# Kernel tuning notes

Measured on AMD Instinct MI355X. Metric: run time of the kernel, lower is better.

The kernel has to match this reference:

```python
import jax, jax.numpy as jnp
from jax import lax
import numpy as np

K = 8          # local window radius -> (2K+1)^2 = 289 offsets
TOPK = 256     # topk channels kept for fg/bg correlation
EPS = 1e-5     # torch InstanceNorm2d default eps


def _conv3(x, w, b):
    # 3x3 conv, stride 1, pad 1, NCHW/OIHW
    y = lax.conv_general_dilated(x, w, (1, 1), ((1, 1), (1, 1)),
                                 dimension_numbers=('NCHW', 'OIHW', 'NCHW'))
    return y + b[None, :, None, None]


def _inorm(x):
    # InstanceNorm2d(affine=False): per (b,c) normalization over HxW, biased var
    m = jnp.mean(x, axis=(2, 3), keepdims=True)
    v = jnp.mean((x - m) ** 2, axis=(2, 3), keepdims=True)
    return (x - m) * lax.rsqrt(v + EPS)


def _aic(x, w1, b1, w2, b2):
    # AIC(in, hidden): conv3x3(in->hidden)+IN+ReLU -> conv3x3(hidden->in)+IN+ReLU
    h = jax.nn.relu(_inorm(_conv3(x, w1, b1)))
    return jax.nn.relu(_inorm(_conv3(h, w2, b2)))


def _amaxpool(x, H, W):
    # adaptive_max_pool2d with exact integer factor (384/48 = 8)
    kh, kw = x.shape[2] // H, x.shape[3] // W
    return lax.reduce_window(x, -jnp.inf, lax.max, (1, 1, kh, kw), (1, 1, kh, kw), 'VALID')


def _topk_c(x, k=TOPK):
    # topk over channel axis, values sorted descending (matches torch.topk)
    v, _ = lax.top_k(jnp.transpose(x, (0, 2, 3, 1)), k)  # [B,H,W,k]
    return jnp.transpose(v, (0, 3, 1, 2))                 # [B,k,H,W]


def _resize_ac(x, H, W):
    # bilinear interpolate, align_corners=True
    B, C, h, w = x.shape
    def grid(n_out, n_in):
        if n_out == 1:
            return jnp.zeros((1,), jnp.float32)
        return jnp.arange(n_out, dtype=jnp.float32) * ((n_in - 1) / (n_out - 1))
    ys, xs = grid(H, h), grid(W, w)
    y0 = jnp.clip(jnp.floor(ys).astype(jnp.int32), 0, h - 1)
    y1 = jnp.minimum(y0 + 1, h - 1)
    x0 = jnp.clip(jnp.floor(xs).astype(jnp.int32), 0, w - 1)
    x1 = jnp.minimum(x0 + 1, w - 1)
    wy = (ys - y0.astype(jnp.float32))[None, None, :, None]
    wx = (xs - x0.astype(jnp.float32))[None, None, None, :]
    rows = x[:, :, y0, :] * (1.0 - wy) + x[:, :, y1, :] * wy  # [B,C,H,w]
    return rows[:, :, :, x0] * (1.0 - wx) + rows[:, :, :, x1] * wx


def _forward(p3, p2, p1, kg1, klp, key_mask, pre_mask,
             conv_top_w, conv_top_b,
             aic_top_w1, aic_top_b1, aic_top_w2, aic_top_b2,
             r1a_w1, r1a_b1, r1a_w2, r1a_b2,
             r1b_w1, r1b_b1, r1b_w2, r1b_b2,
             r2a_w1, r2a_b1, r2a_w2, r2a_b2,
             r2b_w1, r2b_b1, r2b_w2, r2b_b2,
             dec_conv1_w, dec_conv1_b, pred_w, pred_b):
    B, _, H, W = kg1.shape  # kg1: [B, H*W, H, W]
    # --- Global, mode=2: fg/bg topk over the global correlation volume ---
    gm = _amaxpool(key_mask, H, W).reshape(B, H * W, 1, 1)
    gf = _topk_c(kg1 * gm)
    gb = _topk_c(kg1 * (1.0 - gm))
    # --- Local, mode=2: unfold mask into 17x17 windows, fg/bg topk ---
    lm = _amaxpool(pre_mask, H, W)                       # [B,1,H,W]
    lmp = jnp.pad(lm, ((0, 0), (0, 0), (K, K), (K, K)))  # zero pad (FF.pad default)
    patches = lax.conv_general_dilated_patches(
        lmp, (2 * K + 1, 2 * K + 1), (1, 1), 'VALID',
        dimension_numbers=('NCHW', 'OIHW', 'NCHW'))      # [B,289,H,W], ch = dy*17+dx
    lf = _topk_c(klp * patches)
    lb = _topk_c(klp * (1.0 - patches))
    # --- fuse at p3 resolution ---
    pm = _amaxpool(pre_mask, H, W)
    x = jnp.concatenate([p3, gf, gb, lf, lb, pm], axis=1)  # [B, 256*5+1, H, W]
    x = _conv3(x, conv_top_w, conv_top_b)                  # 1281 -> 256
    x = _aic(x, aic_top_w1, aic_top_b1, aic_top_w2, aic_top_b2)
    # --- Decoder: Refine(256,64) -> conv 256->64 -> Refine(64,64) -> pred ---
    y = _resize_ac(x, p2.shape[2], p2.shape[3])
    y = _aic(y, r1a_w1, r1a_b1, r1a_w2, r1a_b2)
    y = y + p2
    y = _aic(y, r1b_w1, r1b_b1, r1b_w2, r1b_b2)
    y = _conv3(y, dec_conv1_w, dec_conv1_b)
    z = _resize_ac(y, p1.shape[2], p1.shape[3])
    z = _aic(z, r2a_w1, r2a_b1, r2a_w2, r2a_b2)
    z = z + p1
    z = _aic(z, r2b_w1, r2b_b1, r2b_w2, r2b_b2)
    return jax.nn.sigmoid(_conv3(z, pred_w, pred_b))       # [B,1,192,192]


def setup_inputs() -> dict:
    key = jax.random.key(0)
    ks = jax.random.split(key, 40)
    B, H, W = 2, 48, 48
    inp = {}
    inp['p3'] = jax.random.normal(ks[0], (B, 256, H, W), jnp.float32)
    inp['p2'] = jax.random.normal(ks[1], (B, 256, 2 * H, 2 * W), jnp.float32)
    inp['p1'] = jax.random.normal(ks[2], (B, 64, 4 * H, 4 * W), jnp.float32)
    inp['kg1'] = jax.random.normal(ks[3], (B, H * W, H, W), jnp.float32)
    inp['klp'] = jax.random.normal(ks[4], (B, (2 * K + 1) ** 2, H, W), jnp.float32)
    inp['key_mask'] = jax.random.uniform(ks[5], (B, 1, 8 * H, 8 * W), dtype=jnp.float32)
    inp['pre_mask'] = jax.random.uniform(ks[6], (B, 1, 8 * H, 8 * W), dtype=jnp.float32)
    i = [7]
    def p(shape, s=0.05):
        w = jax.random.normal(ks[i[0]], shape, jnp.float32) * s
        i[0] += 1
        return w
    inp['conv_top_w'] = p((256, 256 * 5 + 1, 3, 3))
    inp['conv_top_b'] = jnp.zeros((256,), jnp.float32)
    for nm, (ci, ch) in [('aic_top', (256, 64)), ('r1a', (256, 64)), ('r1b', (256, 64)),
                         ('r2a', (64, 64)), ('r2b', (64, 64))]:
        inp[nm + '_w1'] = p((ch, ci, 3, 3)); inp[nm + '_b1'] = jnp.zeros((ch,), jnp.float32)
        inp[nm + '_w2'] = p((ci, ch, 3, 3)); inp[nm + '_b2'] = jnp.zeros((ci,), jnp.float32)
    inp['dec_conv1_w'] = p((64, 256, 3, 3)); inp['dec_conv1_b'] = jnp.zeros((64,), jnp.float32)
    inp['pred_w'] = p((1, 64, 3, 3)); inp['pred_b'] = jnp.zeros((1,), jnp.float32)
    return inp


def reference(p3, p2, p1, kg1, klp, key_mask, pre_mask,
              conv_top_w, conv_top_b,
              aic_top_w1, aic_top_b1, aic_top_w2, aic_top_b2,
              r1a_w1, r1a_b1, r1a_w2, r1a_b2,
              r1b_w1, r1b_b1, r1b_w2, r1b_b2,
              r2a_w1, r2a_b1, r2a_w2, r2a_b2,
              r2b_w1, r2b_b1, r2b_w2, r2b_b2,
              dec_conv1_w, dec_conv1_b, pred_w, pred_b):
    return _forward(p3, p2, p1, kg1, klp, key_mask, pre_mask,
                    conv_top_w, conv_top_b,
                    aic_top_w1, aic_top_b1, aic_top_w2, aic_top_b2,
                    r1a_w1, r1a_b1, r1a_w2, r1a_b2,
                    r1b_w1, r1b_b1, r1b_w2, r1b_b2,
                    r2a_w1, r2a_b1, r2a_w2, r2a_b2,
                    r2b_w1, r2b_b1, r2b_w2, r2b_b2,
                    dec_conv1_w, dec_conv1_b, pred_w, pred_b)
```

## Files before the change

kernel.cpp:

```cpp
#include <hip/hip_runtime.h>
#include <math.h>

#define TPB 256

typedef _Float16 h8 __attribute__((ext_vector_type(8)));
typedef float f4 __attribute__((ext_vector_type(4)));
typedef unsigned short ushort_t;

__device__ __forceinline__ unsigned short f2bf(float x) {
  unsigned int u = __float_as_uint(x);
  unsigned int r = (u + 0x7fffu + ((u >> 16) & 1u)) >> 16;
  return (unsigned short)r;
}
__device__ __forceinline__ float bf2f(unsigned short h) {
  return __uint_as_float(((unsigned int)h) << 16);
}
__device__ __forceinline__ ushort_t f2h(float x) {
  _Float16 h = (_Float16)x;
  return *(ushort_t*)&h;
}
__device__ __forceinline__ float h2f(ushort_t u) {
  _Float16 h = *(_Float16*)&u;
  return (float)h;
}
__device__ __forceinline__ unsigned key_of(float x) {
  unsigned u = __float_as_uint(x);
  return u ^ ((u >> 31) ? 0xFFFFFFFFu : 0x80000000u);
}
__device__ __forceinline__ float un_key(unsigned k) {
  unsigned u = k ^ ((k >> 31) ? 0x80000000u : 0xFFFFFFFFu);
  return __uint_as_float(u);
}

__global__ __launch_bounds__(TPB) void pool8_kernel(const float* __restrict__ in,
                                                    float* __restrict__ out, int total) {
  int idx = blockIdx.x * TPB + threadIdx.x;
  if (idx >= total) return;
  int b = idx / 2304, yx = idx - b * 2304;
  int y = yx / 48, x = yx - y * 48;
  const float* p = in + ((size_t)b * 384 + (size_t)y * 8) * 384 + (size_t)x * 8;
  float m = -INFINITY;
#pragma unroll
  for (int i = 0; i < 8; ++i)
#pragma unroll
    for (int j = 0; j < 8; ++j) m = fmaxf(m, p[(size_t)i * 384 + j]);
  out[idx] = m;
}

__global__ __launch_bounds__(TPB) void tposef_kernel(const float* __restrict__ src,
                                                     float* __restrict__ dst, int C, int HW,
                                                     int DS) {
  __shared__ float tile[64][65];
  int px0 = blockIdx.x * 64;
  int c0 = blockIdx.y * 64;
  int b = blockIdx.z;
  int tid = threadIdx.x;
#pragma unroll
  for (int i = 0; i < 16; ++i) {
    int c = (tid >> 6) + i * 4, p = tid & 63;
    tile[c][p] = src[((size_t)b * C + c0 + c) * HW + px0 + p];
  }
  __syncthreads();
#pragma unroll
  for (int i = 0; i < 16; ++i) {
    int c = tid & 63, p = (tid >> 6) + i * 4;
    dst[((size_t)b * HW + px0 + p) * DS + c0 + c] = tile[c][p];
  }
}

__global__ __launch_bounds__(TPB) void tposeg_kernel(const float* __restrict__ src,
                                                     float* __restrict__ dst, int C, int HW,
                                                     int DS) {
  __shared__ float tile[64][65];
  int px0 = blockIdx.x * 64;
  int c0 = blockIdx.y * 64;
  int b = blockIdx.z;
  int tid = threadIdx.x;
#pragma unroll
  for (int i = 0; i < 16; ++i) {
    int c = (tid >> 6) + i * 4, p = tid & 63;
    float v = 0.f;
    if (c0 + c < C) v = src[((size_t)b * C + c0 + c) * HW + px0 + p];
    tile[c][p] = v;
  }
  __syncthreads();
#pragma unroll
  for (int i = 0; i < 16; ++i) {
    int c = tid & 63, p = (tid >> 6) + i * 4;
    if (c0 + c < C)
      dst[((size_t)b * HW + px0 + p) * DS + c0 + c] = tile[c][p];
  }
}

__global__ __launch_bounds__(TPB) void tposeh_kernel(const float* __restrict__ src,
                                                     ushort_t* __restrict__ dst, int C, int HW,
                                                     int DS) {
  __shared__ float tile[64][65];
  int px0 = blockIdx.x * 64;
  int c0 = blockIdx.y * 64;
  int b = blockIdx.z;
  int tid = threadIdx.x;
#pragma unroll
  for (int i = 0; i < 16; ++i) {
    int c = (tid >> 6) + i * 4, p = tid & 63;
    tile[c][p] = src[((size_t)b * C + c0 + c) * HW + px0 + p];
  }
  __syncthreads();
#pragma unroll
  for (int i = 0; i < 16; ++i) {
    int c = tid & 63, p = (tid >> 6) + i * 4;
    dst[((size_t)b * HW + px0 + p) * DS + c0 + c] = f2h(tile[c][p]);
  }
}

__global__ __launch_bounds__(TPB) void topk_global_kernel(const float* __restrict__ kgT,
                                                          const float* __restrict__ gm,
                                                          ushort_t* __restrict__ xcat) {
  __shared__ unsigned histF[256], histB[256];
  __shared__ unsigned soutF[256], soutB[256];
  __shared__ unsigned selT[2], selA[2];
  __shared__ unsigned cntG[2], cntE[2];
  const int tid = threadIdx.x;
  const int lane = tid & 63, wid = tid >> 6;
  int bid = blockIdx.x;
  int b = bid / 2304, yx = bid - b * 2304;
  const float* kp = kgT + ((size_t)b * 2304 + yx) * 2304;
  const float* gp = gm + (size_t)b * 2304;
  unsigned kF[9], kB[9];
#pragma unroll
  for (int j = 0; j < 9; ++j) {
    int i = tid + 256 * j;
    float v = kp[i];
    float g = gp[i];
    kF[j] = key_of(v * g);
    kB[j] = key_of(v * (1.0f - g));
  }
  unsigned prefF = 0, prefB = 0;
  unsigned KF = 256, KB = 256;
  unsigned gtF = 0, gtB = 0;
#pragma unroll
  for (int p = 0; p < 4; ++p) {
    const int shift = 24 - 8 * p;
    histF[tid] = 0;
    histB[tid] = 0;
    __syncthreads();
#pragma unroll
    for (int j = 0; j < 9; ++j) {
      if (p == 0 || (kF[j] >> (shift + 8)) == prefF)
        atomicAdd(&histF[(kF[j] >> shift) & 0xFFu], 1u);
      if (p == 0 || (kB[j] >> (shift + 8)) == prefB)
        atomicAdd(&histB[(kB[j] >> shift) & 0xFFu], 1u);
    }
    __syncthreads();
    if (wid < 2) {
      unsigned* h = wid ? histB : histF;
      unsigned K = wid ? KB : KF;
      unsigned h0 = h[4 * lane], h1 = h[4 * lane + 1];
      unsigned h2 = h[4 * lane + 2], h3 = h[4 * lane + 3];
      unsigned x = h0 + h1 + h2 + h3;
#pragma unroll
      for (int d = 1; d < 64; d <<= 1) {
        unsigned y = __shfl_down(x, d, 64);
        if (lane + d < 64) x += y;
      }
      unsigned long long m = __ballot(x >= K);
      int tl = 63 - __clzll(m);
      if (lane == tl) {
        unsigned s1 = x - h0, s2 = s1 - h1, s3 = s2 - h2, s4 = s3 - h3;
        int jj;
        unsigned A;
        if (s3 >= K) { jj = 3; A = s4; }
        else if (s2 >= K) { jj = 2; A = s3; }
        else if (s1 >= K) { jj = 1; A = s2; }
        else { jj = 0; A = s1; }
        selT[wid] = 4 * tl + jj;
        selA[wid] = A;
      }
    }
    __syncthreads();
    unsigned TF = selT[0], AF = selA[0];
    unsigned TB = selT[1], AB = selA[1];
    prefF = (prefF << 8) | TF; gtF += AF; KF -= AF;
    prefB = (prefB << 8) | TB; gtB += AB; KB -= AB;
    __syncthreads();
  }
  const unsigned tF = prefF, tB = prefB;
  const unsigned nGTF = gtF, needF = KF;
  const unsigned nGTB = gtB, needB = KB;
  if (tid == 0) { cntG[0] = 0; cntG[1] = 0; cntE[0] = 0; cntE[1] = 0; }
  __syncthreads();
#pragma unroll
  for (int j = 0; j < 9; ++j) {
    unsigned k = kF[j];
    if (k > tF) soutF[atomicAdd(&cntG[0], 1u)] = k;
    else if (k == tF) {
      unsigned e = atomicAdd(&cntE[0], 1u);
      if (e < needF) soutF[nGTF + e] = tF;
    }
    k = kB[j];
    if (k > tB) soutB[atomicAdd(&cntG[1], 1u)] = k;
    else if (k == tB) {
      unsigned e = atomicAdd(&cntE[1], 1u);
      if (e < needB) soutB[nGTB + e] = tB;
    }
  }
  __syncthreads();
  if (wid < 2) {
    unsigned* sarr = wid ? soutB : soutF;
    for (int kk = 2; kk <= 256; kk <<= 1) {
      for (int j = kk >> 1; j > 0; j >>= 1) {
#pragma unroll
        for (int r = 0; r < 2; ++r) {
          int p = lane + r * 64;
          int t = (p & (j - 1)) | ((p & ~(j - 1)) << 1);
          int ixj = t | j;
          bool up = ((t & kk) == 0);
          unsigned a = sarr[t], c = sarr[ixj];
          if (up ? (a > c) : (a < c)) { sarr[t] = c; sarr[ixj] = a; }
        }
        __builtin_amdgcn_wave_barrier();
      }
    }
  }
  __syncthreads();
  size_t base = ((size_t)(b * 2304 + yx)) * 1312;
  xcat[base + 256 + tid] = f2h(un_key(soutF[255 - tid]));
  xcat[base + 512 + tid] = f2h(un_key(soutB[255 - tid]));
}

__global__ __launch_bounds__(64) void topk_local_kernel(const float* __restrict__ klpT,
                                                        const float* __restrict__ lm,
                                                        ushort_t* __restrict__ xcat) {
  __shared__ float sf[512];
  __shared__ float sb[512];
  const int lane = threadIdx.x;
  const int pix = blockIdx.x;
  const int b = pix / 2304;
  const int yx = pix - b * 2304;
  const int y = yx / 48, x = yx - y * 48;
  const float* kp = klpT + (size_t)pix * 320;
#pragma unroll
  for (int r = 0; r < 8; ++r) {
    int i = lane + r * 64;
    float vf = -INFINITY, vb = -INFINITY;
    if (i < 289) {
      int dy = i / 17, dx = i - dy * 17;
      int sy = y + dy - 8, sx = x + dx - 8;
      float pv = 0.f;
      if (sy >= 0 && sy < 48 && sx >= 0 && sx < 48) pv = lm[(size_t)b * 2304 + sy * 48 + sx];
      float v = kp[i];
      vf = v * pv;
      vb = v * (1.0f - pv);
    }
    sf[i] = vf;
    sb[i] = vb;
  }
  __builtin_amdgcn_wave_barrier();
  for (int k = 2; k <= 512; k <<= 1) {
    for (int j = k >> 1; j > 0; j >>= 1) {
#pragma unroll
      for (int r = 0; r < 4; ++r) {
        int p = lane + r * 64;
        int t = (p & (j - 1)) | ((p & ~(j - 1)) << 1);
        int ixj = t | j;
        bool up = ((t & k) == 0);
        float a = sf[t], c = sf[ixj];
        if (up ? (a > c) : (a < c)) { sf[t] = c; sf[ixj] = a; }
        a = sb[t]; c = sb[ixj];
        if (up ? (a > c) : (a < c)) { sb[t] = c; sb[ixj] = a; }
      }
      __builtin_amdgcn_wave_barrier();
    }
  }
  size_t base = (size_t)pix * 1312;
#pragma unroll
  for (int r = 0; r < 4; ++r) {
    int t = lane + r * 64;
    xcat[base + 768 + t] = f2h(sf[511 - t]);
    xcat[base + 1024 + t] = f2h(sb[511 - t]);
  }
}

__global__ __launch_bounds__(TPB) void pm_pad_kernel(const float* __restrict__ lm,
                                                     ushort_t* __restrict__ xcat) {
  int idx = blockIdx.x * TPB + threadIdx.x;
  if (idx >= 2 * 2304 * 32) return;
  int ch = idx & 31;
  int r = idx >> 5;
  xcat[(size_t)r * 1312 + 1280 + ch] = (ch == 0) ? f2h(lm[r]) : (ushort_t)0;
}

struct WallDesc {
  const float* src[13];
  int CinW[13], CIP[13], CoutPad[13], CoutReal[13];
  unsigned start[14];
  int n;
};
__global__ __launch_bounds__(TPB) void wconv_all_kernel(WallDesc D, ushort_t* __restrict__ whi,
                                                        int total) {
  int i = blockIdx.x * TPB + threadIdx.x;
  if (i >= total) return;
  int k = 0;
  while (k + 1 < D.n && (unsigned)i >= D.start[k + 1]) ++k;
  int j = i - D.start[k];
  int e = j & 7;
  int t = j >> 3;
  int l16 = t & 15; t >>= 4;
  int h4 = t & 3; t >>= 2;
  int NCOG = D.CoutPad[k] >> 4;
  int cog = t % NCOG; t /= NCOG;
  int kykx = t % 9;
  int chunk = t / 9;
  int co = cog * 16 + l16;
  int ci = chunk * 32 + h4 * 8 + e;
  float v = 0.f;
  if (ci < D.CinW[k] && co < D.CoutReal[k])
    v = D.src[k][((size_t)co * D.CinW[k] + ci) * 9 + kykx];
  whi[i] = f2h(v);
}

template <int NORM>
__device__ __forceinline__ uint4 norm8(uint4 v, const float* __restrict__ nmean,
                                       const float* __restrict__ ninv,
                                       const void* __restrict__ nres, size_t mb,
                                       size_t pxoff) {
  float f[8];
  f[0] = h2f((ushort_t)(v.x & 0xffff)); f[1] = h2f((ushort_t)(v.x >> 16));
  f[2] = h2f((ushort_t)(v.y & 0xffff)); f[3] = h2f((ushort_t)(v.y >> 16));
  f[4] = h2f((ushort_t)(v.z & 0xffff)); f[5] = h2f((ushort_t)(v.z >> 16));
  f[6] = h2f((ushort_t)(v.w & 0xffff)); f[7] = h2f((ushort_t)(v.w >> 16));
  float4 m0 = *(const float4*)(nmean + mb);
  float4 m1 = *(const float4*)(nmean + mb + 4);
  float4 i0 = *(const float4*)(ninv + mb);
  float4 i1 = *(const float4*)(ninv + mb + 4);
  float o[8];
  o[0] = fmaxf((f[0] - m0.x) * i0.x, 0.f);
  o[1] = fmaxf((f[1] - m0.y) * i0.y, 0.f);
  o[2] = fmaxf((f[2] - m0.z) * i0.z, 0.f);
  o[3] = fmaxf((f[3] - m0.w) * i0.w, 0.f);
  o[4] = fmaxf((f[4] - m1.x) * i1.x, 0.f);
  o[5] = fmaxf((f[5] - m1.y) * i1.y, 0.f);
  o[6] = fmaxf((f[6] - m1.z) * i1.z, 0.f);
  o[7] = fmaxf((f[7] - m1.w) * i1.w, 0.f);
  if (NORM == 2) {
    uint4 rv = *(const uint4*)((const ushort_t*)nres + pxoff);
    o[0] += h2f((ushort_t)(rv.x & 0xffff)); o[1] += h2f((ushort_t)(rv.x >> 16));
    o[2] += h2f((ushort_t)(rv.y & 0xffff)); o[3] += h2f((ushort_t)(rv.y >> 16));
    o[4] += h2f((ushort_t)(rv.z & 0xffff)); o[5] += h2f((ushort_t)(rv.z >> 16));
    o[6] += h2f((ushort_t)(rv.w & 0xffff)); o[7] += h2f((ushort_t)(rv.w >> 16));
  } else if (NORM == 3) {
    const float* rp = (const float*)nres + pxoff;
    float4 r0 = *(const float4*)rp;
    float4 r1 = *(const float4*)(rp + 4);
    o[0] += r0.x; o[1] += r0.y; o[2] += r0.z; o[3] += r0.w;
    o[4] += r1.x; o[5] += r1.y; o[6] += r1.z; o[7] += r1.w;
  }
  uint4 out;
  out.x = (unsigned)f2h(o[0]) | ((unsigned)f2h(o[1]) << 16);
  out.y = (unsigned)f2h(o[2]) | ((unsigned)f2h(o[3]) << 16);
  out.z = (unsigned)f2h(o[4]) | ((unsigned)f2h(o[5]) << 16);
  out.w = (unsigned)f2h(o[6]) | ((unsigned)f2h(o[7]) << 16);
  return out;
}

template <int MFR, int ACT, int STAT, int GEOM, int NORM>
__global__ __launch_bounds__(TPB) void conv_mfma_kernel(
    const ushort_t* __restrict__ in, const ushort_t* __restrict__ whi,
    const float* __restrict__ bias,
    ushort_t* __restrict__ outh, float* __restrict__ outf, ushort_t* __restrict__ partial,
    float* __restrict__ stat, int ntiles,
    const float* __restrict__ nmean, const float* __restrict__ ninv,
    const void* __restrict__ nres,
    int hin, int win, float rs,
    int CIP, int Cout, int H, int W, int S, int ci_per_s) {
  const int NPIX = (GEOM == 1) ? 100 : 180;
  const int PITCH = 10;
  __shared__ uint4 sB[(GEOM == 1) ? 800 : 1440];
  const int MB = (GEOM == 1) ? 64 : MFR * 32;
  const int tid = threadIdx.x;
  const int lane = tid & 63;
  const int lo16 = lane & 15, hi4 = lane >> 4;
  const int wid = tid >> 6;
  const int wco = (GEOM == 1) ? wid : (wid & 1);
  const int wpx = (GEOM == 1) ? 0 : (wid >> 1);
  const int tilesX = W >> 3;
  const int tx0 = (blockIdx.x % tilesX) << 3;
  const int ty0 = (blockIdx.x / tilesX) << ((GEOM == 1) ? 3 : 4);
  const int s = blockIdx.y % S;
  const int co0 = (blockIdx.y / S) * MB;
  const int b = blockIdx.z;
  const int NCOG = Cout >> 4;
  const size_t HW = (size_t)H * W;
  const ushort_t* inb = in + (size_t)b * HW * CIP;
  const ushort_t* srcb = in + (size_t)b * hin * win * CIP;
  int ci_begin = s * ci_per_s;
  int ci_end = ci_begin + ci_per_s;
  if (ci_end > CIP) ci_end = CIP;
  f4 acc[MFR][4];
#pragma unroll
  for (int m = 0; m < MFR; ++m)
#pragma unroll
    for (int n = 0; n < 4; ++n) acc[m][n] = (f4){0.f, 0.f, 0.f, 0.f};

  for (int ci0 = ci_begin; ci0 < ci_end; ci0 += 64) {
    const bool has2 = (ci0 + 32 < ci_end);
    __syncthreads();
#pragma unroll
    for (int it = 0; it < 6; ++it) {
      int u = it * TPB + tid;
      if (u < NPIX * 8) {
        int q4 = u / NPIX;
        int pix = u - q4 * NPIX;
        int prow = pix / PITCH, pcol = pix - prow * PITCH;
        int gy = ty0 - 1 + prow, gx = tx0 - 1 + pcol;
        int ci = ci0 + q4 * 8;
        bool inbp = (ci < CIP && gy >= 0 && gy < H && gx >= 0 && gx < W);
        uint4 v = {0u, 0u, 0u, 0u};
        if (inbp) {
          if (NORM <= 3) {
            v = *(const uint4*)(inb + ((size_t)gy * W + gx) * CIP + ci);
            if (NORM != 0) {
              size_t mb = (size_t)b * CIP + ci;
              size_t pxoff = ((size_t)b * HW + (size_t)gy * W + gx) * CIP + ci;
              v = norm8<NORM>(v, nmean, ninv, nres, mb, pxoff);
            }
          } else {
            float ys = gy * rs, xs = gx * rs;
            int y0 = (int)floorf(ys);
            if (y0 > hin - 1) y0 = hin - 1;
            int x0 = (int)floorf(xs);
            if (x0 > win - 1) x0 = win - 1;
            int y1 = y0 + 1 < hin ? y0 + 1 : hin - 1;
            int x1 = x0 + 1 < win ? x0 + 1 : win - 1;
            float wy = ys - (float)y0, wx = xs - (float)x0;
            uint4 s00 = *(const uint4*)(srcb + ((size_t)y0 * win + x0) * CIP + ci);
            uint4 s01 = *(const uint4*)(srcb + ((size_t)y0 * win + x1) * CIP + ci);
            uint4 s10 = *(const uint4*)(srcb + ((size_t)y1 * win + x0) * CIP + ci);
            uint4 s11 = *(const uint4*)(srcb + ((size_t)y1 * win + x1) * CIP + ci);
            float w00 = (1.f - wy) * (1.f - wx), w01 = (1.f - wy) * wx;
            float w10 = wy * (1.f - wx), w11 = wy * wx;
            union U8 { uint4 q; ushort_t sv[8]; };
            U8 u00, u01, u10, u11, uo;
            u00.q = s00; u01.q = s01; u10.q = s10; u11.q = s11;
#pragma unroll
            for (int k8 = 0; k8 < 8; ++k8) {
              float val = h2f(u00.sv[k8]) * w00 + h2f(u01.sv[k8]) * w01 +
                          h2f(u10.sv[k8]) * w10 + h2f(u11.sv[k8]) * w11;
              uo.sv[k8] = f2h(val);
            }
            v = uo.q;
          }
        }
        sB[q4 * NPIX + pix] = v;
      }
    }
    __syncthreads();
#pragma unroll
    for (int h = 0; h < 2; ++h) {
      if (h == 1 && !has2) continue;
      const int chunkIdx = (ci0 >> 5) + h;
#pragma unroll
      for (int ky = 0; ky < 3; ++ky) {
#pragma unroll
        for (int kx = 0; kx < 3; ++kx) {
          const int kykx = ky * 3 + kx;
          h8 ah[MFR];
#pragma unroll
          for (int m = 0; m < MFR; ++m) {
            int cog = (co0 + wco * (GEOM == 1 ? 16 : (MB / 2)) + m * 16) >> 4;
            size_t woff = (((size_t)chunkIdx * 9 + kykx) * NCOG + cog) * 512 + (size_t)lane * 8;
            ah[m] = *(const h8*)(whi + woff);
          }
          h8 bf[4];
#pragma unroll
          for (int n = 0; n < 4; ++n) {
            int pix = (wpx * 8 + n * 2 + (lo16 >> 3) + ky) * PITCH + (lo16 & 7) + kx;
            union { uint4 q; h8 v; } ub;
            ub.q = sB[(h * 4 + hi4) * NPIX + pix];
            bf[n] = ub.v;
          }
#pragma unroll
          for (int m = 0; m < MFR; ++m)
#pragma unroll
            for (int n = 0; n < 4; ++n)
              acc[m][n] = __builtin_amdgcn_mfma_f32_16x16x32_f16(ah[m], bf[n], acc[m][n], 0, 0, 0);
        }
      }
    }
  }

#pragma unroll
  for (int m = 0; m < MFR; ++m) {
#pragma unroll
    for (int n = 0; n < 4; ++n) {
      int py = ty0 + wpx * 8 + n * 2 + (lo16 >> 3);
      int pxx = tx0 + (lo16 & 7);
      int co_r0 = co0 + wco * (GEOM == 1 ? 16 : (MB / 2)) + m * 16 + hi4 * 4;
      if (ACT == 1) {
        if (wco == 0 && m == 0 && hi4 == 0) {
          float v = acc[0][n][0] + bias[0];
          outf[(size_t)b * HW + (size_t)py * W + pxx] = 1.0f / (1.0f + expf(-v));
        }
      } else if (S == 1) {
        float4 bv = *(const float4*)(bias + co_r0);
        unsigned w0 = (unsigned)f2h(acc[m][n][0] + bv.x) |
                      ((unsigned)f2h(acc[m][n][1] + bv.y) << 16);
        unsigned w1 = (unsigned)f2h(acc[m][n][2] + bv.z) |
                      ((unsigned)f2h(acc[m][n][3] + bv.w) << 16);
        uint2 o = {w0, w1};
        *(uint2*)(outh + (((size_t)b * HW + (size_t)py * W + pxx) * Cout + co_r0)) = o;
        if (STAT) {
          acc[m][n][0] = h2f((ushort_t)(w0 & 0xffff));
          acc[m][n][1] = h2f((ushort_t)(w0 >> 16));
          acc[m][n][2] = h2f((ushort_t)(w1 & 0xffff));
          acc[m][n][3] = h2f((ushort_t)(w1 >> 16));
        }
      } else {
        uint2 o;
        o.x = (unsigned)f2h(acc[m][n][0]) | ((unsigned)f2h(acc[m][n][1]) << 16);
        o.y = (unsigned)f2h(acc[m][n][2]) | ((unsigned)f2h(acc[m][n][3]) << 16);
        *(uint2*)(partial + (((size_t)(s * 2 + b) * HW + (size_t)py * W + pxx) * Cout + co_r0)) = o;
      }
    }
  }

  if (STAT) {
    __syncthreads();
    f4* lredS = (f4*)sB;
    f4* lredQ = lredS + 32;
    if (GEOM == 1) {
// ... 549 lines not shown
```

Before: 534.5 us.

## Radix-select global top-k on fp16 keys with two passes and per-wave histograms

The global top-k now converts products to fp16 order-preserving 16-bit keys before selection, cutting the radix select from four 8-bit passes to two. The first pass uses per-wave histograms to reduce shared-memory atomic contention, and the sort buffers become 16-bit. Because the output was already stored as fp16, selection on fp16 keys gives the same values, though ties caused by fp16 rounding can shift which elements are picked but not the output values.

```diff
diff --git a/kernel.cpp b/kernel.cpp
--- a/kernel.cpp
+++ b/kernel.cpp
@@ -23,13 +23,12 @@
   _Float16 h = *(_Float16*)&u;
   return (float)h;
 }
-__device__ __forceinline__ unsigned key_of(float x) {
-  unsigned u = __float_as_uint(x);
-  return u ^ ((u >> 31) ? 0xFFFFFFFFu : 0x80000000u);
-}
-__device__ __forceinline__ float un_key(unsigned k) {
-  unsigned u = k ^ ((k >> 31) ? 0x80000000u : 0xFFFFFFFFu);
-  return __uint_as_float(u);
+__device__ __forceinline__ unsigned key16_of(float x) {
+  unsigned h = (unsigned)f2h(x);
+  return h ^ ((h >> 15) ? 0xFFFFu : 0x8000u);
+}
+__device__ __forceinline__ ushort_t un_key16(unsigned k) {
+  return (ushort_t)(k ^ ((k & 0x8000u) ? 0x8000u : 0xFFFFu));
 }
 
 __global__ __launch_bounds__(TPB) void pool8_kernel(const float* __restrict__ in,
@@ -116,8 +115,8 @@
 __global__ __launch_bounds__(TPB) void topk_global_kernel(const float* __restrict__ kgT,
                                                           const float* __restrict__ gm,
                                                           ushort_t* __restrict__ xcat) {
-  __shared__ unsigned histF[256], histB[256];
-  __shared__ unsigned soutF[256], soutB[256];
+  __shared__ unsigned histF[4][256], histB[4][256];
+  __shared__ ushort_t soutF[256], soutB[256];
   __shared__ unsigned selT[2], selA[2];
   __shared__ unsigned cntG[2], cntE[2];
   const int tid = threadIdx.x;
@@ -132,81 +131,113 @@
     int i = tid + 256 * j;
     float v = kp[i];
     float g = gp[i];
-    kF[j] = key_of(v * g);
-    kB[j] = key_of(v * (1.0f - g));
-  }
-  unsigned prefF = 0, prefB = 0;
-  unsigned KF = 256, KB = 256;
-  unsigned gtF = 0, gtB = 0;
-#pragma unroll
-  for (int p = 0; p < 4; ++p) {
-    const int shift = 24 - 8 * p;
-    histF[tid] = 0;
-    histB[tid] = 0;
-    __syncthreads();
-#pragma unroll
-    for (int j = 0; j < 9; ++j) {
-      if (p == 0 || (kF[j] >> (shift + 8)) == prefF)
-        atomicAdd(&histF[(kF[j] >> shift) & 0xFFu], 1u);
-      if (p == 0 || (kB[j] >> (shift + 8)) == prefB)
-        atomicAdd(&histB[(kB[j] >> shift) & 0xFFu], 1u);
-    }
-    __syncthreads();
-    if (wid < 2) {
-      unsigned* h = wid ? histB : histF;
-      unsigned K = wid ? KB : KF;
-      unsigned h0 = h[4 * lane], h1 = h[4 * lane + 1];
-      unsigned h2 = h[4 * lane + 2], h3 = h[4 * lane + 3];
-      unsigned x = h0 + h1 + h2 + h3;
-#pragma unroll
-      for (int d = 1; d < 64; d <<= 1) {
-        unsigned y = __shfl_down(x, d, 64);
-        if (lane + d < 64) x += y;
-      }
-      unsigned long long m = __ballot(x >= K);
-      int tl = 63 - __clzll(m);
-      if (lane == tl) {
-        unsigned s1 = x - h0, s2 = s1 - h1, s3 = s2 - h2, s4 = s3 - h3;
-        int jj;
-        unsigned A;
-        if (s3 >= K) { jj = 3; A = s4; }
-        else if (s2 >= K) { jj = 2; A = s3; }
-        else if (s1 >= K) { jj = 1; A = s2; }
-        else { jj = 0; A = s1; }
-        selT[wid] = 4 * tl + jj;
-        selA[wid] = A;
-      }
-    }
-    __syncthreads();
-    unsigned TF = selT[0], AF = selA[0];
-    unsigned TB = selT[1], AB = selA[1];
-    prefF = (prefF << 8) | TF; gtF += AF; KF -= AF;
-    prefB = (prefB << 8) | TB; gtB += AB; KB -= AB;
-    __syncthreads();
-  }
-  const unsigned tF = prefF, tB = prefB;
-  const unsigned nGTF = gtF, needF = KF;
-  const unsigned nGTB = gtB, needB = KB;
+    kF[j] = key16_of(v * g);
+    kB[j] = key16_of(v * (1.0f - g));
+  }
+#pragma unroll
+  for (int w = 0; w < 4; ++w) {
+    histF[w][tid] = 0;
+    histB[w][tid] = 0;
+  }
+  __syncthreads();
+#pragma unroll
+  for (int j = 0; j < 9; ++j) {
+    atomicAdd(&histF[wid][kF[j] >> 8], 1u);
+    atomicAdd(&histB[wid][kB[j] >> 8], 1u);
+  }
+  __syncthreads();
+  if (wid < 2) {
+    unsigned(*hh)[256] = wid ? histB : histF;
+    unsigned h0 = hh[0][4 * lane] + hh[1][4 * lane] + hh[2][4 * lane] + hh[3][4 * lane];
+    unsigned h1 = hh[0][4 * lane + 1] + hh[1][4 * lane + 1] + hh[2][4 * lane + 1] +
+                  hh[3][4 * lane + 1];
+    unsigned h2 = hh[0][4 * lane + 2] + hh[1][4 * lane + 2] + hh[2][4 * lane + 2] +
+                  hh[3][4 * lane + 2];
+    unsigned h3 = hh[0][4 * lane + 3] + hh[1][4 * lane + 3] + hh[2][4 * lane + 3] +
+                  hh[3][4 * lane + 3];
+    unsigned x = h0 + h1 + h2 + h3;
+#pragma unroll
+    for (int d = 1; d < 64; d <<= 1) {
+      unsigned y = __shfl_down(x, d, 64);
+      if (lane + d < 64) x += y;
+    }
+    unsigned long long m = __ballot(x >= 256u);
+    int tl = 63 - __clzll(m);
+    if (lane == tl) {
+      unsigned s1 = x - h0, s2 = s1 - h1, s3 = s2 - h2, s4 = s3 - h3;
+      int jj;
+      unsigned A;
+      if (s3 >= 256u) { jj = 3; A = s4; }
+      else if (s2 >= 256u) { jj = 2; A = s3; }
+      else if (s1 >= 256u) { jj = 1; A = s2; }
+      else { jj = 0; A = s1; }
+      selT[wid] = 4 * tl + jj;
+      selA[wid] = A;
+    }
+  }
+  __syncthreads();
+  const unsigned T0F = selT[0], gt0F = selA[0];
+  const unsigned T0B = selT[1], gt0B = selA[1];
+  const unsigned KF = 256u - gt0F, KB = 256u - gt0B;
+  histF[0][tid] = 0;
+  histB[0][tid] = 0;
+  __syncthreads();
+#pragma unroll
+  for (int j = 0; j < 9; ++j) {
+    if ((kF[j] >> 8) == T0F) atomicAdd(&histF[0][kF[j] & 0xFFu], 1u);
+    if ((kB[j] >> 8) == T0B) atomicAdd(&histB[0][kB[j] & 0xFFu], 1u);
+  }
+  __syncthreads();
+  if (wid < 2) {
+    unsigned* h = wid ? histB[0] : histF[0];
+    unsigned K = wid ? KB : KF;
+    unsigned h0 = h[4 * lane], h1 = h[4 * lane + 1];
+    unsigned h2 = h[4 * lane + 2], h3 = h[4 * lane + 3];
+    unsigned x = h0 + h1 + h2 + h3;
+#pragma unroll
+    for (int d = 1; d < 64; d <<= 1) {
+      unsigned y = __shfl_down(x, d, 64);
+      if (lane + d < 64) x += y;
+    }
+    unsigned long long m = __ballot(x >= K);
+    int tl = 63 - __clzll(m);
+    if (lane == tl) {
+      unsigned s1 = x - h0, s2 = s1 - h1, s3 = s2 - h2, s4 = s3 - h3;
+      int jj;
+      unsigned A;
+      if (s3 >= K) { jj = 3; A = s4; }
+      else if (s2 >= K) { jj = 2; A = s3; }
+      else if (s1 >= K) { jj = 1; A = s2; }
+      else { jj = 0; A = s1; }
+      selT[wid] = 4 * tl + jj;
+      selA[wid] = A;
+    }
+  }
+  __syncthreads();
+  const unsigned tF = (T0F << 8) | selT[0];
+  const unsigned tB = (T0B << 8) | selT[1];
+  const unsigned nGTF = gt0F + selA[0], needF = 256u - nGTF;
+  const unsigned nGTB = gt0B + selA[1], needB = 256u - nGTB;
   if (tid == 0) { cntG[0] = 0; cntG[1] = 0; cntE[0] = 0; cntE[1] = 0; }
   __syncthreads();
 #pragma unroll
   for (int j = 0; j < 9; ++j) {
     unsigned k = kF[j];
-    if (k > tF) soutF[atomicAdd(&cntG[0], 1u)] = k;
+    if (k > tF) soutF[atomicAdd(&cntG[0], 1u)] = (ushort_t)k;
     else if (k == tF) {
       unsigned e = atomicAdd(&cntE[0], 1u);
-      if (e < needF) soutF[nGTF + e] = tF;
+      if (e < needF) soutF[nGTF + e] = (ushort_t)tF;
     }
     k = kB[j];
-    if (k > tB) soutB[atomicAdd(&cntG[1], 1u)] = k;
+    if (k > tB) soutB[atomicAdd(&cntG[1], 1u)] = (ushort_t)k;
     else if (k == tB) {
       unsigned e = atomicAdd(&cntE[1], 1u);
-      if (e < needB) soutB[nGTB + e] = tB;
+      if (e < needB) soutB[nGTB + e] = (ushort_t)tB;
     }
   }
   __syncthreads();
   if (wid < 2) {
-    unsigned* sarr = wid ? soutB : soutF;
+    ushort_t* sarr = wid ? soutB : soutF;
     for (int kk = 2; kk <= 256; kk <<= 1) {
       for (int j = kk >> 1; j > 0; j >>= 1) {
 #pragma unroll
@@ -215,7 +246,7 @@
           int t = (p & (j - 1)) | ((p & ~(j - 1)) << 1);
           int ixj = t | j;
           bool up = ((t & kk) == 0);
-          unsigned a = sarr[t], c = sarr[ixj];
+          ushort_t a = sarr[t], c = sarr[ixj];
           if (up ? (a > c) : (a < c)) { sarr[t] = c; sarr[ixj] = a; }
         }
         __builtin_amdgcn_wave_barrier();
@@ -224,8 +255,8 @@
   }
   __syncthreads();
   size_t base = ((size_t)(b * 2304 + yx)) * 1312;
-  xcat[base + 256 + tid] = f2h(un_key(soutF[255 - tid]));
-  xcat[base + 512 + tid] = f2h(un_key(soutB[255 - tid]));
+  xcat[base + 256 + tid] = un_key16((unsigned)soutF[255 - tid]);
+  xcat[base + 512 + tid] = un_key16((unsigned)soutB[255 - tid]);
 }
 
 __global__ __launch_bounds__(64) void topk_local_kernel(const float* __restrict__ klpT,
```

Result: faster. 517.6 us (-3.2%).
